# Kernel optimization log

Measured on AMD Instinct MI355X. Metric: run time of the kernel, lower is better.

The kernel has to match this reference:

```python
import jax, jax.numpy as jnp
import numpy as np

NNODES = 16384
DIM = 512
ALPHA = 3.0
K = 10  # min(scale_hyperedges=10, nnodes)


def setup_inputs() -> dict:
    key = jax.random.key(0)
    k1, k2, k3 = jax.random.split(key, 3)
    return {
        "idx": jnp.arange(NNODES, dtype=jnp.int32),
        # nn.Embedding default init: N(0, 1)
        "emb_weight": jax.random.normal(k1, (NNODES, DIM), dtype=jnp.float32),
        # nn.Linear default init scale ~ 1/sqrt(fan_in)
        "lin_w": jax.random.uniform(k2, (DIM, DIM), dtype=jnp.float32,
                                    minval=-1.0, maxval=1.0) / np.float32(np.sqrt(DIM)),
        "lin_b": jax.random.uniform(k3, (DIM,), dtype=jnp.float32,
                                    minval=-1.0, maxval=1.0) / np.float32(np.sqrt(DIM)),
    }


def reference(idx, emb_weight, lin_w, lin_b):
    # node_features = emb1(idx)                      [N, D]
    feats = emb_weight[idx]
    # transformed = tanh(alpha * lin1(feats))        [N, D]
    t = jnp.tanh(ALPHA * (feats @ lin_w.T + lin_b))
    # sim = T @ T^T                                  [N, N]
    sim = t @ t.T
    # top-k most similar nodes per row
    _, top_idx = jax.lax.top_k(sim, K)               # [N, K]
    n = emb_weight.shape[0]
    rows = jnp.arange(n)[:, None]                    # [N, 1]
    # H[i, top_idx[i]] = 1, then transpose -> incidence [nodes, hyperedges]
    H = jnp.zeros((n, n), dtype=t.dtype).at[rows, top_idx].set(1.0)
    return H.T
```

## Files before the change

### kernel.cpp

```cpp
#include <hip/hip_runtime.h>
#include <hip/hip_bf16.h>
#include <math.h>

#define NN 16384
#define DD 512
#define KSEL 10
#define MCAND 8
#define NSPLIT 8
#define NPANEL 128
#define RESCORE 16

typedef __bf16 bf16x8 __attribute__((ext_vector_type(8)));
typedef float  f32x4  __attribute__((ext_vector_type(4)));

#define GLOAD_LDS16(gsrc, ldst) \
    __builtin_amdgcn_global_load_lds( \
        (const __attribute__((address_space(1))) void*)(gsrc), \
        (__attribute__((address_space(3))) void*)(ldst), 16, 0, 0)

__global__ __launch_bounds__(256) void k_transform(
    const int* __restrict__ idx, const float* __restrict__ emb,
    const float* __restrict__ W, const float* __restrict__ bias,
    float* __restrict__ t_out, unsigned short* __restrict__ tb_out)
{
    __shared__ float As[32][68];
    __shared__ float Bs[32][68];
    const int tid = threadIdx.x;
    const int tx = tid & 15, ty = tid >> 4;
    const int m0 = (blockIdx.x >> 3) << 6;
    const int n0 = (blockIdx.x & 7) << 6;

    float acc[4][4] = {};

    const int f0 = tid, f1 = tid + 256;
    const int r0 = f0 >> 3, c0_ = f0 & 7;
    const int r1 = f1 >> 3, c1_ = f1 & 7;
    const int ga0 = idx[m0 + r0];
    const int ga1 = idx[m0 + r1];

    for (int kc = 0; kc < DD; kc += 32) {
        const float4 a0 = *(const float4*)&emb[(size_t)ga0 * DD + kc + (c0_ << 2)];
        const float4 a1 = *(const float4*)&emb[(size_t)ga1 * DD + kc + (c1_ << 2)];
        const float4 b0 = *(const float4*)&W[(size_t)(n0 + r0) * DD + kc + (c0_ << 2)];
        const float4 b1 = *(const float4*)&W[(size_t)(n0 + r1) * DD + kc + (c1_ << 2)];
        As[(c0_<<2)+0][r0] = a0.x; As[(c0_<<2)+1][r0] = a0.y;
        As[(c0_<<2)+2][r0] = a0.z; As[(c0_<<2)+3][r0] = a0.w;
        As[(c1_<<2)+0][r1] = a1.x; As[(c1_<<2)+1][r1] = a1.y;
        As[(c1_<<2)+2][r1] = a1.z; As[(c1_<<2)+3][r1] = a1.w;
        Bs[(c0_<<2)+0][r0] = b0.x; Bs[(c0_<<2)+1][r0] = b0.y;
        Bs[(c0_<<2)+2][r0] = b0.z; Bs[(c0_<<2)+3][r0] = b0.w;
        Bs[(c1_<<2)+0][r1] = b1.x; Bs[(c1_<<2)+1][r1] = b1.y;
        Bs[(c1_<<2)+2][r1] = b1.z; Bs[(c1_<<2)+3][r1] = b1.w;
        __syncthreads();
        #pragma unroll
        for (int k = 0; k < 32; ++k) {
            const float4 a = *(const float4*)&As[k][ty << 2];
            const float4 b = *(const float4*)&Bs[k][tx << 2];
            const float av[4] = {a.x, a.y, a.z, a.w};
            const float bv[4] = {b.x, b.y, b.z, b.w};
            #pragma unroll
            for (int i = 0; i < 4; ++i)
                #pragma unroll
                for (int j = 0; j < 4; ++j)
                    acc[i][j] = fmaf(av[i], bv[j], acc[i][j]);
        }
        __syncthreads();
    }

    #pragma unroll
    for (int i = 0; i < 4; ++i) {
        const int m = m0 + (ty << 2) + i;
        float o[4];
        union { __hip_bfloat16 h[4]; ushort4 u; } cc;
        #pragma unroll
        for (int j = 0; j < 4; ++j) {
            const int n = n0 + (tx << 2) + j;
            o[j] = tanhf(3.0f * (acc[i][j] + bias[n]));
            cc.h[j] = __float2bfloat16(o[j]);
        }
        *(float4*)&t_out[(size_t)m * DD + n0 + (tx << 2)] =
            make_float4(o[0], o[1], o[2], o[3]);
        *(ushort4*)&tb_out[(size_t)m * DD + n0 + (tx << 2)] = cc.u;
    }
}

__global__ __launch_bounds__(256) void k_sim_topk(
    const unsigned short* __restrict__ tb,
    float* __restrict__ pv, unsigned short* __restrict__ pi)
{
    __shared__ __align__(16) char SM[56320];
    float*          topv   = (float*)(SM + 49152);
    unsigned short* topi   = (unsigned short*)(SM + 53248);
    float*          thresh = (float*)(SM + 55296);
    int*            cnt    = (int*)(SM + 55808);
    float*          cv     = (float*)(SM);
    int*            ci     = (int*)(SM + 16896);

    const int tid  = threadIdx.x;
    const int wave = tid >> 6;
    const int lane = tid & 63;
    const int wr   = wave >> 1;
    const int wc   = wave & 1;

    const int bid  = blockIdx.x;
    const int s    = bid & 7;
    const int mblk = bid >> 3;
    const int m0   = mblk << 7;
    const int c_begin = s * (NN / NSPLIT);

    if (tid < 128) {
        thresh[tid] = -1e30f;
        cnt[tid] = 0;
        #pragma unroll
        for (int j = 0; j < MCAND; ++j) { topv[tid*MCAND + j] = -1e30f; topi[tid*MCAND + j] = 0xFFFFu; }
    }
    __syncthreads();

    const char* tbb = (const char*)tb;
    const int l4r = lane >> 2;
    const int l4u = lane & 3;

    for (int ct = 0; ct < (NN / NSPLIT) / 128; ++ct) {
        const int c0 = c_begin + (ct << 7);
        f32x4 acc[4][4] = {};

        auto STAGE = [&](int k) {
            const int rb = k % 3;
            const size_t kb = (size_t)k << 6;
            char* Ad = SM + rb * 16384;
            char* Bd = Ad + 8192;
            #pragma unroll
            for (int i_ = 0; i_ < 2; ++i_) {
                const int ai = (wave << 1) + i_;
                const int rl = (ai << 4) + l4r;
                GLOAD_LDS16(tbb + (size_t)(m0 + rl) * 1024 + kb + ((size_t)(l4u ^ ((rl >> 1) & 3)) << 4),
                            Ad + (ai << 10));
                GLOAD_LDS16(tbb + (size_t)(c0 + rl) * 1024 + kb + ((size_t)(l4u ^ ((rl >> 1) & 3)) << 4),
                            Bd + (ai << 10));
            }
        };

        auto COMPUTE = [&](int k) {
            const int rb = k % 3;
            const char* Ac = SM + rb * 16384;
            const char* Bc = Ac + 8192;
            const int u = lane >> 4;
            bf16x8 af[4], bf[4];
            #pragma unroll
            for (int m = 0; m < 4; ++m) {
                const int row = (wr << 6) + (m << 4) + (lane & 15);
                af[m] = *(const bf16x8*)(Ac + (row << 6) + ((u ^ ((row >> 1) & 3)) << 4));
            }
            #pragma unroll
            for (int n = 0; n < 4; ++n) {
                const int row = (wc << 6) + (n << 4) + (lane & 15);
                bf[n] = *(const bf16x8*)(Bc + (row << 6) + ((u ^ ((row >> 1) & 3)) << 4));
            }
            #pragma unroll
            for (int m = 0; m < 4; ++m)
                #pragma unroll
                for (int n = 0; n < 4; ++n)
                    acc[m][n] = __builtin_amdgcn_mfma_f32_16x16x32_bf16(
                        af[m], bf[n], acc[m][n], 0, 0, 0);
        };

        STAGE(0); STAGE(1);
        for (int kc = 0; kc < 14; ++kc) {
            asm volatile("s_waitcnt vmcnt(4)" ::: "memory");
            __builtin_amdgcn_s_barrier();
            STAGE(kc + 2);
            COMPUTE(kc);
        }
        asm volatile("s_waitcnt vmcnt(4)" ::: "memory");
        __builtin_amdgcn_s_barrier();
        COMPUTE(14);
        asm volatile("s_waitcnt vmcnt(0)" ::: "memory");
        __builtin_amdgcn_s_barrier();
        COMPUTE(15);

        __syncthreads();

        #pragma unroll
        for (int rnd = 0; rnd < 4; ++rnd) {
            const int wcr = rnd >> 1;
            const int nf0 = (rnd & 1) << 1;
            if (wc == wcr) {
                #pragma unroll
                for (int m = 0; m < 4; ++m) {
                    #pragma unroll
                    for (int nn = 0; nn < 2; ++nn) {
                        #pragma unroll
                        for (int j = 0; j < 4; ++j) {
                            const int row = (wr << 6) + (m << 4) + ((lane >> 4) << 2) + j;
                            const float v = acc[m][nf0 + nn][j];
                            if (v >= thresh[row]) {
                                const int p = atomicAdd(&cnt[row], 1);
                                cv[row * 33 + p] = v;
                                ci[row * 33 + p] = c0 + (wcr << 6) + ((nf0 + nn) << 4) + (lane & 15);
                            }
                        }
                    }
                }
            }
            __syncthreads();
            if (tid < 128) {
                const int r = tid;
                const int n_ = cnt[r];
                float* tv = &topv[r * MCAND];
                unsigned short* ti = &topi[r * MCAND];
                for (int q = 0; q < n_; ++q) {
                    const float v = cv[r * 33 + q];
                    const unsigned short c = (unsigned short)ci[r * 33 + q];
                    if (v > tv[MCAND-1] || (v == tv[MCAND-1] && c < ti[MCAND-1])) {
                        int p = MCAND - 1;
                        while (p > 0 && (v > tv[p-1] || (v == tv[p-1] && c < ti[p-1]))) {
                            tv[p] = tv[p-1]; ti[p] = ti[p-1]; --p;
                        }
                        tv[p] = v; ti[p] = c;
                    }
                }
                cnt[r] = 0;
                thresh[r] = tv[MCAND-1];
            }
            __syncthreads();
        }
    }

    if (tid < 128) {
        const size_t base = (((size_t)s * NPANEL + mblk) * 128 + tid) * MCAND;
        #pragma unroll
        for (int j = 0; j < MCAND; ++j) {
            pv[base + j] = topv[tid * MCAND + j];
            pi[base + j] = topi[tid * MCAND + j];
        }
    }
}

__global__ __launch_bounds__(256) void k_rescore(
    const float* __restrict__ t, const float* __restrict__ pv,
    const unsigned short* __restrict__ pi, float* __restrict__ out)
{
    const int wave = threadIdx.x >> 6;
    const int lane = threadIdx.x & 63;
    const int r = blockIdx.x * 4 + wave;
    const int panel = r >> 7, local = r & 127;

    const int sp = lane >> 3, slot = lane & 7;
    const size_t cbase = (((size_t)sp * NPANEL + panel) * 128 + local) * MCAND;
    const float v = pv[cbase + slot];
    const unsigned int idxc = pi[cbase + slot];
    const unsigned int u = __float_as_uint(v);
    const unsigned int mkey = (u & 0x80000000u) ? ~u : (u | 0x80000000u);
    unsigned long long key = ((unsigned long long)mkey << 16) |
                             (unsigned long long)((~idxc) & 0xFFFFu);

    #pragma unroll
    for (int k = 2; k <= 64; k <<= 1) {
        #pragma unroll
        for (int j = k >> 1; j > 0; j >>= 1) {
            const unsigned long long other = __shfl_xor(key, j, 64);
            const bool lower = (lane & j) == 0;
            const bool ascBlock = (lane & k) == 0;
            const bool takeMax = (lower == ascBlock);
            const bool mineBigger = key > other;
            key = (takeMax == mineBigger) ? key : other;
        }
    }
    const int cid = (int)((~(unsigned int)key) & 0xFFFFu);

    const float4 a0 = *(const float4*)&t[(size_t)r * DD + lane * 8];
    const float4 a1 = *(const float4*)&t[(size_t)r * DD + lane * 8 + 4];

    double bestv[KSEL];
    int    besti[KSEL];
    #pragma unroll
    for (int j = 0; j < KSEL; ++j) { bestv[j] = -1e300; besti[j] = 0x7fffffff; }

    for (int q = 0; q < RESCORE; ++q) {
        const int c = __shfl(cid, q, 64);
        const float4 v0 = *(const float4*)&t[(size_t)c * DD + lane * 8];
        const float4 v1 = *(const float4*)&t[(size_t)c * DD + lane * 8 + 4];
        double sdot = 0.0;
        sdot += (double)a0.x * (double)v0.x;
        sdot += (double)a0.y * (double)v0.y;
        sdot += (double)a0.z * (double)v0.z;
        sdot += (double)a0.w * (double)v0.w;
        sdot += (double)a1.x * (double)v1.x;
        sdot += (double)a1.y * (double)v1.y;
        sdot += (double)a1.z * (double)v1.z;
        sdot += (double)a1.w * (double)v1.w;
        #pragma unroll
        for (int off = 32; off > 0; off >>= 1)
            sdot += __shfl_down(sdot, off, 64);
        if (lane == 0) {
            if (sdot > bestv[KSEL-1] || (sdot == bestv[KSEL-1] && c < besti[KSEL-1])) {
                int p = KSEL - 1;
                while (p > 0 && (sdot > bestv[p-1] ||
                                 (sdot == bestv[p-1] && c < besti[p-1]))) {
                    bestv[p] = bestv[p-1]; besti[p] = besti[p-1]; --p;
                }
                bestv[p] = sdot; besti[p] = c;
            }
        }
    }

    if (lane == 0) {
        #pragma unroll
        for (int j = 0; j < KSEL; ++j)
            out[(size_t)besti[j] * NN + r] = 1.0f;
    }
}

extern "C" void kernel_launch(void* const* d_in, const int* in_sizes, int n_in,
                              void* d_out, int out_size, void* d_ws, size_t ws_size,
                              hipStream_t stream) {
    const int*   idx  = (const int*)d_in[0];
    const float* emb  = (const float*)d_in[1];
    const float* linw = (const float*)d_in[2];
    const float* linb = (const float*)d_in[3];
    float* out = (float*)d_out;

    float*          t  = (float*)d_ws;
    unsigned short* tb = (unsigned short*)((char*)d_ws + (size_t)32 * 1024 * 1024);
    float*          pv = (float*)((char*)d_ws + (size_t)48 * 1024 * 1024);
    unsigned short* pi = (unsigned short*)((char*)d_ws + (size_t)52 * 1024 * 1024);

    (void)hipMemsetAsync(d_out, 0, (size_t)NN * (size_t)NN * sizeof(float), stream);

    k_transform<<<dim3(256 * 8), dim3(256), 0, stream>>>(idx, emb, linw, linb, t, tb);
    k_sim_topk<<<dim3(NPANEL * NSPLIT), dim3(256), 0, stream>>>(tb, pv, pi);
    k_rescore<<<dim3(NN / 4), dim3(256), 0, stream>>>(t, pv, pi, out);
}
```

Baseline: 2.618 ms.

## Keep full A row-panel resident in LDS across column tiles in sim-topk

The kernel now loads the block's full 128x512 bf16 A panel into LDS once, using an XOR swizzle, instead of re-streaming A for every 128-column tile. Only B is triple-buffered per k-step, which halves global loads in the main loop and reduces the vmcnt wait depth. LDS use grows to about 159 KB, which limits occupancy to one block per CU. The candidate buffer is reorganised into 8 rounds of 16 columns so that it fits alongside the panel, at the cost of more barriers and top-k merge passes.

```diff
diff --git a/kernel.cpp b/kernel.cpp
--- a/kernel.cpp
+++ b/kernel.cpp
@@ -88,13 +88,13 @@
     const unsigned short* __restrict__ tb,
     float* __restrict__ pv, unsigned short* __restrict__ pi)
 {
-    __shared__ __align__(16) char SM[56320];
-    float*          topv   = (float*)(SM + 49152);
-    unsigned short* topi   = (unsigned short*)(SM + 53248);
-    float*          thresh = (float*)(SM + 55296);
-    int*            cnt    = (int*)(SM + 55808);
-    float*          cv     = (float*)(SM);
-    int*            ci     = (int*)(SM + 16896);
+    __shared__ __align__(16) char SM[162816];
+    float*          topv   = (float*)(SM + 155648);
+    unsigned short* topi   = (unsigned short*)(SM + 159744);
+    float*          thresh = (float*)(SM + 161792);
+    int*            cnt    = (int*)(SM + 162304);
+    float*          cv     = (float*)(SM + 131072);
+    int*            ci     = (int*)(SM + 139776);
 
     const int tid  = threadIdx.x;
     const int wave = tid >> 6;
@@ -114,47 +114,48 @@
         #pragma unroll
         for (int j = 0; j < MCAND; ++j) { topv[tid*MCAND + j] = -1e30f; topi[tid*MCAND + j] = 0xFFFFu; }
     }
+
+    const char* tbb = (const char*)tb;
+
+    for (int i = 0; i < 32; ++i) {
+        const int rl = (wave << 5) + i;
+        GLOAD_LDS16(tbb + (size_t)(m0 + rl) * 1024 + (size_t)((lane << 4) ^ ((rl & 7) << 4)),
+                    SM + (rl << 10));
+    }
+    asm volatile("s_waitcnt vmcnt(0)" ::: "memory");
     __syncthreads();
-
-    const char* tbb = (const char*)tb;
-    const int l4r = lane >> 2;
-    const int l4u = lane & 3;
 
     for (int ct = 0; ct < (NN / NSPLIT) / 128; ++ct) {
         const int c0 = c_begin + (ct << 7);
         f32x4 acc[4][4] = {};
 
-        auto STAGE = [&](int k) {
-            const int rb = k % 3;
+        auto STAGE_B = [&](int k) {
+            char* Bd = SM + 131072 + (k % 3) * 8192;
             const size_t kb = (size_t)k << 6;
-            char* Ad = SM + rb * 16384;
-            char* Bd = Ad + 8192;
             #pragma unroll
             for (int i_ = 0; i_ < 2; ++i_) {
-                const int ai = (wave << 1) + i_;
-                const int rl = (ai << 4) + l4r;
-                GLOAD_LDS16(tbb + (size_t)(m0 + rl) * 1024 + kb + ((size_t)(l4u ^ ((rl >> 1) & 3)) << 4),
-                            Ad + (ai << 10));
-                GLOAD_LDS16(tbb + (size_t)(c0 + rl) * 1024 + kb + ((size_t)(l4u ^ ((rl >> 1) & 3)) << 4),
-                            Bd + (ai << 10));
+                const int instr = (wave << 1) + i_;
+                const int rl = (instr << 4) + (lane >> 2);
+                GLOAD_LDS16(tbb + (size_t)(c0 + rl) * 1024 + kb
+                                + (size_t)((((lane & 3) << 4)) ^ ((rl & 3) << 4)),
+                            Bd + (instr << 10));
             }
         };
 
-        auto COMPUTE = [&](int k) {
-            const int rb = k % 3;
-            const char* Ac = SM + rb * 16384;
-            const char* Bc = Ac + 8192;
+        auto COMPUTE = [&](int kc) {
+            const char* Bc = SM + 131072 + (kc % 3) * 8192;
             const int u = lane >> 4;
             bf16x8 af[4], bf[4];
             #pragma unroll
             for (int m = 0; m < 4; ++m) {
                 const int row = (wr << 6) + (m << 4) + (lane & 15);
-                af[m] = *(const bf16x8*)(Ac + (row << 6) + ((u ^ ((row >> 1) & 3)) << 4));
+                af[m] = *(const bf16x8*)(SM + (row << 10)
+                        + (((kc << 6) + (u << 4)) ^ ((row & 7) << 4)));
             }
             #pragma unroll
             for (int n = 0; n < 4; ++n) {
                 const int row = (wc << 6) + (n << 4) + (lane & 15);
-                bf[n] = *(const bf16x8*)(Bc + (row << 6) + ((u ^ ((row >> 1) & 3)) << 4));
+                bf[n] = *(const bf16x8*)(Bc + (row << 6) + ((u ^ (row & 3)) << 4));
             }
             #pragma unroll
             for (int m = 0; m < 4; ++m)
@@ -164,14 +165,14 @@
                         af[m], bf[n], acc[m][n], 0, 0, 0);
         };
 
-        STAGE(0); STAGE(1);
+        STAGE_B(0); STAGE_B(1);
         for (int kc = 0; kc < 14; ++kc) {
-            asm volatile("s_waitcnt vmcnt(4)" ::: "memory");
+            asm volatile("s_waitcnt vmcnt(2)" ::: "memory");
             __builtin_amdgcn_s_barrier();
-            STAGE(kc + 2);
+            STAGE_B(kc + 2);
             COMPUTE(kc);
         }
-        asm volatile("s_waitcnt vmcnt(4)" ::: "memory");
+        asm volatile("s_waitcnt vmcnt(2)" ::: "memory");
         __builtin_amdgcn_s_barrier();
         COMPUTE(14);
         asm volatile("s_waitcnt vmcnt(0)" ::: "memory");
@@ -181,23 +182,20 @@
         __syncthreads();
 
         #pragma unroll
-        for (int rnd = 0; rnd < 4; ++rnd) {
-            const int wcr = rnd >> 1;
-            const int nf0 = (rnd & 1) << 1;
+        for (int rnd = 0; rnd < 8; ++rnd) {
+            const int wcr = rnd >> 2;
+            const int nf = rnd & 3;
             if (wc == wcr) {
                 #pragma unroll
                 for (int m = 0; m < 4; ++m) {
                     #pragma unroll
-                    for (int nn = 0; nn < 2; ++nn) {
-                        #pragma unroll
-                        for (int j = 0; j < 4; ++j) {
-                            const int row = (wr << 6) + (m << 4) + ((lane >> 4) << 2) + j;
-                            const float v = acc[m][nf0 + nn][j];
-                            if (v >= thresh[row]) {
-                                const int p = atomicAdd(&cnt[row], 1);
-                                cv[row * 33 + p] = v;
-                                ci[row * 33 + p] = c0 + (wcr << 6) + ((nf0 + nn) << 4) + (lane & 15);
-                            }
+                    for (int j = 0; j < 4; ++j) {
+                        const int row = (wr << 6) + (m << 4) + ((lane >> 4) << 2) + j;
+                        const float v = acc[m][nf][j];
+                        if (v >= thresh[row]) {
+                            const int p = atomicAdd(&cnt[row], 1);
+                            cv[row * 17 + p] = v;
+                            ci[row * 17 + p] = c0 + (wcr << 6) + (nf << 4) + (lane & 15);
                         }
                     }
                 }
@@ -209,8 +207,8 @@
                 float* tv = &topv[r * MCAND];
                 unsigned short* ti = &topi[r * MCAND];
                 for (int q = 0; q < n_; ++q) {
-                    const float v = cv[r * 33 + q];
-                    const unsigned short c = (unsigned short)ci[r * 33 + q];
+                    const float v = cv[r * 17 + q];
+                    const unsigned short c = (unsigned short)ci[r * 17 + q];
                     if (v > tv[MCAND-1] || (v == tv[MCAND-1] && c < ti[MCAND-1])) {
                         int p = MCAND - 1;
                         while (p > 0 && (v > tv[p-1] || (v == tv[p-1] && c < ti[p-1]))) {
```

After: 2.815 ms. 1.08x slower.
